# Kernel optimization log

Hardware: AMD Instinct MI355X
Metric: run time of the kernel (lower is better)

The kernel has to match this reference:

```python
import jax, jax.numpy as jnp
import numpy as np

N_NODES = 100000
N_EDGES = 1600000
NFEAT = 256
NHID = 128


def _l2_normalize(v, eps=1e-12):
    return v / (jnp.linalg.norm(v) + eps)


def setup_inputs() -> dict:
    key = jax.random.key(0)
    k1, k2, k3, k4 = jax.random.split(key, 4)
    x = jax.random.normal(k1, (N_NODES, NFEAT), dtype=jnp.float32)
    edge_index = jax.random.randint(k2, (2, N_EDGES), 0, N_NODES, dtype=jnp.int64)
    # GCNConv weight (glorot-ish scale), spectral-normalized at forward time
    W = jax.random.normal(k3, (NFEAT, NHID), dtype=jnp.float32) * 0.05
    bias = jnp.zeros((NHID,), dtype=jnp.float32)
    prelu_a = jnp.full((1,), 0.25, dtype=jnp.float32)  # nn.PReLU default slope
    u = _l2_normalize(jax.random.normal(k4, (NFEAT,), dtype=jnp.float32))
    return {"x": x, "edge_index": edge_index, "W": W, "bias": bias,
            "prelu_a": prelu_a, "u": u}


def reference(x, edge_index, W, bias, prelu_a, u):
    # --- spectral_norm: one power iteration (torch default n_power_iterations=1) ---
    v = _l2_normalize(W.T @ u)          # [NHID]
    u2 = _l2_normalize(W @ v)           # [NFEAT]
    sigma = u2 @ (W @ v)
    W_sn = W / sigma

    # --- GCNConv: linear transform, add self-loops, sym-normalize, scatter-add ---
    xw = x @ W_sn                       # [N, NHID]
    n = x.shape[0]
    loops = jnp.arange(n, dtype=edge_index.dtype)
    row = jnp.concatenate([edge_index[0], loops])  # sources
    col = jnp.concatenate([edge_index[1], loops])  # targets
    ones = jnp.ones(row.shape[0], dtype=x.dtype)
    deg = jax.ops.segment_sum(ones, col, num_segments=n)
    dinv = jnp.where(deg > 0, deg ** -0.5, 0.0)
    norm = dinv[row] * dinv[col]        # [E+N]
    msgs = norm[:, None] * xw[row]      # gather at sources
    out = jax.ops.segment_sum(msgs, col, num_segments=n) + bias

    # --- PReLU ---
    return jnp.where(out > 0, out, prelu_a * out)
```

## Files before the change

### kernel.cpp

```cpp
#include <hip/hip_runtime.h>

#define NFEAT 256
#define NHID  128

#define NBK   391
#define EPB   4096
#define NBLK  391
#define SEGW  4608

typedef __bf16 bf16x8 __attribute__((ext_vector_type(8)));
typedef __bf16 bf16x4 __attribute__((ext_vector_type(4)));
typedef float  f32x4  __attribute__((ext_vector_type(4)));

#define PIN() __builtin_amdgcn_sched_barrier(0)

__global__ __launch_bounds__(256) void sigma_kernel(const float* __restrict__ W,
                                                    const float* __restrict__ u,
                                                    float* __restrict__ scal,
                                                    int* __restrict__ bucket_fill) {
    __shared__ float v[NHID];
    __shared__ float red[256];
    int tid = threadIdx.x;

    if (tid < NBK) bucket_fill[tid] = 0;
    if (tid + 256 < NBK) bucket_fill[tid + 256] = 0;

    float t = 0.f;
    if (tid < NHID) {
        for (int i = 0; i < NFEAT; ++i) t += W[i * NHID + tid] * u[i];
    }
    red[tid] = (tid < NHID) ? t * t : 0.f;
    __syncthreads();
    for (int s = 128; s > 0; s >>= 1) {
        if (tid < s) red[tid] += red[tid + s];
        __syncthreads();
    }
    float nv = sqrtf(red[0]);
    float inv_nv = 1.f / (nv + 1e-12f);
    __syncthreads();
    if (tid < NHID) v[tid] = t * inv_nv;
    __syncthreads();

    float wv = 0.f;
    for (int j = 0; j < NHID; ++j) wv += W[tid * NHID + j] * v[j];
    red[tid] = wv * wv;
    __syncthreads();
    for (int s = 128; s > 0; s >>= 1) {
        if (tid < s) red[tid] += red[tid + s];
        __syncthreads();
    }
    if (tid == 0) {
        float n2  = red[0];
        float nwv = sqrtf(n2);
        float sigma = n2 / (nwv + 1e-12f);
        scal[0] = 1.f / sigma;
    }
}

__global__ __launch_bounds__(256) void wt_kernel(const float* __restrict__ W,
                                                 const float* __restrict__ scal,
                                                 __bf16* __restrict__ WT) {
    int idx = blockIdx.x * 256 + threadIdx.x;
    int c = idx >> 8;
    int r = idx & 255;
    WT[c * NFEAT + r] = (__bf16)(W[r * NHID + c] * scal[0]);
}

__global__ __launch_bounds__(256) void fused_kernel(const float* __restrict__ x,
                                                    const __bf16* __restrict__ WT,
                                                    __bf16* __restrict__ xwb,
                                                    const int* __restrict__ erow,
                                                    const int* __restrict__ ecol,
                                                    int* __restrict__ bucket_fill,
                                                    unsigned int* __restrict__ rbuf,
                                                    int nn, int E, int ngemm) {
    __shared__ __attribute__((aligned(16))) char sbuf[49152];

    int tid  = threadIdx.x;

    if ((int)blockIdx.x < ngemm) {
        float (*xs)[64][64] = (float (*)[64][64])sbuf;

        int lane = tid & 63;
        int w    = tid >> 6;
        int rfrag = lane & 15;
        int kg    = lane >> 4;
        int row0 = blockIdx.x * 64;

        int p16  = lane & 15;
        int rsub = lane >> 4;

        int crow0 = (w & 1) * 32 + rfrag;
        int col0  = (w >> 1) * 64;
        int r0 = row0 + crow0;
        int r1 = r0 + 16;
        const __bf16* wb = WT + (size_t)(col0 + rfrag) * NFEAT + kg * 8;
        int cr7 = crow0 & 7;

        f32x4 acc0[4] = {};
        f32x4 acc1[4] = {};

        auto STAGE = [&](int buf, int c) {
#pragma unroll
            for (int j = 0; j < 4; ++j) {
                int rloc = w * 16 + j * 4 + rsub;
                int grow = row0 + rloc;
                if (grow >= nn) grow = nn - 1;
                const float* src = x + (size_t)grow * NFEAT + c * 64 + ((p16 ^ (grow & 7)) << 2);
                __builtin_amdgcn_global_load_lds(
                    (const __attribute__((address_space(1))) void*)src,
                    (__attribute__((address_space(3))) void*)&xs[buf][w * 16 + j * 4][0],
                    16, 0, 0);
            }
        };

        bf16x8 Bf[2][2][4];
        auto BLOAD = [&](int bbuf, int c) {
#pragma unroll
            for (int ks = 0; ks < 2; ++ks)
#pragma unroll
                for (int nt = 0; nt < 4; ++nt)
                    Bf[bbuf][ks][nt] = *(const bf16x8*)(wb + (size_t)nt * 16 * NFEAT + c * 64 + ks * 32);
        };

        auto MFMA_CHUNK = [&](int buf, int bbuf) {
#pragma unroll
            for (int ks = 0; ks < 2; ++ks) {
                int sA = kg * 2 + ks * 8;
                float4 a0lo = *(const float4*)&xs[buf][crow0][((sA) ^ cr7) * 4];
                float4 a0hi = *(const float4*)&xs[buf][crow0][((sA + 1) ^ cr7) * 4];
                float4 a1lo = *(const float4*)&xs[buf][crow0 + 16][((sA) ^ cr7) * 4];
                float4 a1hi = *(const float4*)&xs[buf][crow0 + 16][((sA + 1) ^ cr7) * 4];
                bf16x8 af0, af1;
                af0[0] = (__bf16)a0lo.x; af0[1] = (__bf16)a0lo.y;
                af0[2] = (__bf16)a0lo.z; af0[3] = (__bf16)a0lo.w;
                af0[4] = (__bf16)a0hi.x; af0[5] = (__bf16)a0hi.y;
                af0[6] = (__bf16)a0hi.z; af0[7] = (__bf16)a0hi.w;
                af1[0] = (__bf16)a1lo.x; af1[1] = (__bf16)a1lo.y;
                af1[2] = (__bf16)a1lo.z; af1[3] = (__bf16)a1lo.w;
                af1[4] = (__bf16)a1hi.x; af1[5] = (__bf16)a1hi.y;
                af1[6] = (__bf16)a1hi.z; af1[7] = (__bf16)a1hi.w;
#pragma unroll
                for (int nt = 0; nt < 4; ++nt) {
                    acc0[nt] = __builtin_amdgcn_mfma_f32_16x16x32_bf16(Bf[bbuf][ks][nt], af0, acc0[nt], 0, 0, 0);
                    acc1[nt] = __builtin_amdgcn_mfma_f32_16x16x32_bf16(Bf[bbuf][ks][nt], af1, acc1[nt], 0, 0, 0);
                }
            }
        };

        STAGE(0, 0);  PIN();
        BLOAD(0, 0);  PIN();
        STAGE(1, 1);  PIN();
        asm volatile("s_waitcnt vmcnt(12)" ::: "memory");
        __builtin_amdgcn_s_barrier();

        BLOAD(1, 1);  PIN();
        STAGE(2, 2);  PIN();
        MFMA_CHUNK(0, 0);
        asm volatile("s_waitcnt vmcnt(12)" ::: "memory");
        __builtin_amdgcn_s_barrier();

        BLOAD(0, 2);  PIN();
        STAGE(0, 3);  PIN();
        MFMA_CHUNK(1, 1);
        asm volatile("s_waitcnt vmcnt(12)" ::: "memory");
        __builtin_amdgcn_s_barrier();

        BLOAD(1, 3);  PIN();
        MFMA_CHUNK(2, 0);
        asm volatile("s_waitcnt vmcnt(8)" ::: "memory");
        __builtin_amdgcn_s_barrier();

        MFMA_CHUNK(0, 1);

        if (r0 < nn) {
            __bf16* orow = xwb + (size_t)r0 * NHID + col0 + kg * 4;
#pragma unroll
            for (int nt = 0; nt < 4; ++nt) {
                bf16x4 v;
                v[0] = (__bf16)acc0[nt][0];
                v[1] = (__bf16)acc0[nt][1];
                v[2] = (__bf16)acc0[nt][2];
                v[3] = (__bf16)acc0[nt][3];
                *(bf16x4*)&orow[nt * 16] = v;
            }
        }
        if (r1 < nn) {
            __bf16* orow = xwb + (size_t)r1 * NHID + col0 + kg * 4;
#pragma unroll
            for (int nt = 0; nt < 4; ++nt) {
                bf16x4 v;
                v[0] = (__bf16)acc1[nt][0];
                v[1] = (__bf16)acc1[nt][1];
                v[2] = (__bf16)acc1[nt][2];
                v[3] = (__bf16)acc1[nt][3];
                *(bf16x4*)&orow[nt * 16] = v;
            }
        }
        return;
    }

    unsigned int*   rec   = (unsigned int*)sbuf;
    unsigned short* bkk   = (unsigned short*)(sbuf + 16384);
    int*            hist  = (int*)(sbuf + 24576);
    int*            lbase = (int*)(sbuf + 24576 + 1564);
    int*            lfill = (int*)(sbuf + 24576 + 3128);
    int*            gb    = (int*)(sbuf + 24576 + 4692);

    int b = blockIdx.x - ngemm;
    for (int k = tid; k < NBK; k += 256) { hist[k] = 0; lfill[k] = 0; }
    __syncthreads();

    int e0 = b * EPB;
    unsigned int rv[16];
    int kv[16];
#pragma unroll
    for (int j = 0; j < 16; ++j) {
        int idx = e0 + j * 256 + tid;
        if (idx < E) {
            int c = ecol[idx];
            int s = erow[idx];
            int k = c >> 8;
            kv[j] = k;
            rv[j] = ((unsigned int)(c & 255) << 24) | (unsigned int)s;
            atomicAdd(&hist[k], 1);
        } else kv[j] = -1;
    }
    __syncthreads();

    if (tid < 64) {
        int carry = 0;
        for (int c0 = 0; c0 < NBK; c0 += 64) {
            int i = c0 + tid;
            int vv = (i < NBK) ? hist[i] : 0;
            int orig = vv;
#pragma unroll
            for (int d = 1; d < 64; d <<= 1) {
                int t = __shfl_up(vv, (unsigned)d, 64);
                if (tid >= d) vv += t;
            }
            if (i < NBK) lbase[i] = carry + vv - orig;
            carry += __shfl(vv, 63, 64);
        }
    }
    __syncthreads();

    if (tid < NBK) gb[tid] = tid * SEGW + atomicAdd(&bucket_fill[tid], hist[tid]);
    if (tid + 256 < NBK) gb[tid + 256] = (tid + 256) * SEGW
                                       + atomicAdd(&bucket_fill[tid + 256], hist[tid + 256]);
    __syncthreads();

#pragma unroll
    for (int j = 0; j < 16; ++j) {
        if (kv[j] >= 0) {
            int p = lbase[kv[j]] + atomicAdd(&lfill[kv[j]], 1);
            rec[p] = rv[j];
            bkk[p] = (unsigned short)kv[j];
        }
    }
    __syncthreads();

    int nval = E - e0;
    if (nval > EPB) nval = EPB;
    for (int p = tid; p < nval; p += 256) {
        int k = bkk[p];
        rbuf[gb[k] + (p - lbase[k])] = rec[p];
    }
}

__global__ __launch_bounds__(256) void fine_kernel(const unsigned int* __restrict__ rbuf,
                                                   const int* __restrict__ bucket_fill,
                                                   int4* __restrict__ meta,
                                                   float* __restrict__ dinv,
                                                   int* __restrict__ ebuf, int n) {
    __shared__ int cnt[256], lb[256], lf[256], sc[256];
    int tid = threadIdx.x, k = blockIdx.x;
    int seg0 = k * SEGW, seg1 = seg0 + bucket_fill[k];
    cnt[tid] = 0;
    lf[tid] = 0;
    __syncthreads();
    for (int j = seg0 + tid; j < seg1; j += 256)
        atomicAdd(&cnt[rbuf[j] >> 24], 1);
    __syncthreads();
    int cv = cnt[tid];
    sc[tid] = cv;
    __syncthreads();
    int val = cv;
    for (int off = 1; off < 256; off <<= 1) {
        int t = (tid >= off) ? sc[tid - off] : 0;
        __syncthreads();
        val += t;
        sc[tid] = val;
        __syncthreads();
    }
    lb[tid] = val - cv;
    __syncthreads();
    int node = k * 256 + tid;
    if (node < n) {
        float dv = rsqrtf((float)cv + 1.f);
        int4 m;
        m.x = seg0 + lb[tid];
        m.y = cv;
        m.z = __float_as_int(dv);
        m.w = 0;
        meta[node] = m;
        dinv[node] = dv;
    }
    for (int j = seg0 + tid; j < seg1; j += 256) {
        unsigned int r = rbuf[j];
        int dl = r >> 24;
        int p = seg0 + lb[dl] + atomicAdd(&lf[dl], 1);
        ebuf[p] = (int)(r & 0xFFFFFFu);
    }
}

__global__ __launch_bounds__(256) void gather_kernel(const uint4* __restrict__ xb4,
                                                     const int4* __restrict__ meta,
                                                     const int* __restrict__ ebuf,
                                                     const float* __restrict__ dinv,
                                                     const float* __restrict__ bias,
                                                     const float* __restrict__ pa,
                                                     float* __restrict__ out, int n) {
    int tid = threadIdx.x;
    int sub = tid & 15;
    int node = (blockIdx.x * 256 + tid) >> 4;
    if (node >= n) return;

    int4 m = meta[node];
    int b = m.x, deg = m.y;
    float dn = __int_as_float(m.z);

    uint4 s0 = xb4[(size_t)node * 16 + sub];
    float a0 = dn * __uint_as_float(s0.x << 16);
    float a1 = dn * __uint_as_float(s0.x & 0xffff0000u);
    float a2 = dn * __uint_as_float(s0.y << 16);
    float a3 = dn * __uint_as_float(s0.y & 0xffff0000u);
    float a4 = dn * __uint_as_float(s0.z << 16);
    float a5 = dn * __uint_as_float(s0.z & 0xffff0000u);
    float a6 = dn * __uint_as_float(s0.w << 16);
    float a7 = dn * __uint_as_float(s0.w & 0xffff0000u);

    int k = 0;
    for (; k + 4 <= deg; k += 4) {
        int r0 = ebuf[b + k + 0];
        int r1 = ebuf[b + k + 1];
        int r2 = ebuf[b + k + 2];
        int r3 = ebuf[b + k + 3];
        float d0 = dinv[r0], d1 = dinv[r1], d2 = dinv[r2], d3 = dinv[r3];
        uint4 v0 = xb4[(size_t)r0 * 16 + sub];
        uint4 v1 = xb4[(size_t)r1 * 16 + sub];
        uint4 v2 = xb4[(size_t)r2 * 16 + sub];
        uint4 v3 = xb4[(size_t)r3 * 16 + sub];
        a0 += d0 * __uint_as_float(v0.x << 16) + d1 * __uint_as_float(v1.x << 16)
            + d2 * __uint_as_float(v2.x << 16) + d3 * __uint_as_float(v3.x << 16);
        a1 += d0 * __uint_as_float(v0.x & 0xffff0000u) + d1 * __uint_as_float(v1.x & 0xffff0000u)
            + d2 * __uint_as_float(v2.x & 0xffff0000u) + d3 * __uint_as_float(v3.x & 0xffff0000u);
        a2 += d0 * __uint_as_float(v0.y << 16) + d1 * __uint_as_float(v1.y << 16)
            + d2 * __uint_as_float(v2.y << 16) + d3 * __uint_as_float(v3.y << 16);
        a3 += d0 * __uint_as_float(v0.y & 0xffff0000u) + d1 * __uint_as_float(v1.y & 0xffff0000u)
            + d2 * __uint_as_float(v2.y & 0xffff0000u) + d3 * __uint_as_float(v3.y & 0xffff0000u);
        a4 += d0 * __uint_as_float(v0.z << 16) + d1 * __uint_as_float(v1.z << 16)
            + d2 * __uint_as_float(v2.z << 16) + d3 * __uint_as_float(v3.z << 16);
        a5 += d0 * __uint_as_float(v0.z & 0xffff0000u) + d1 * __uint_as_float(v1.z & 0xffff0000u)
            + d2 * __uint_as_float(v2.z & 0xffff0000u) + d3 * __uint_as_float(v3.z & 0xffff0000u);
        a6 += d0 * __uint_as_float(v0.w << 16) + d1 * __uint_as_float(v1.w << 16)
            + d2 * __uint_as_float(v2.w << 16) + d3 * __uint_as_float(v3.w << 16);
        a7 += d0 * __uint_as_float(v0.w & 0xffff0000u) + d1 * __uint_as_float(v1.w & 0xffff0000u)
            + d2 * __uint_as_float(v2.w & 0xffff0000u) + d3 * __uint_as_float(v3.w & 0xffff0000u);
    }
    for (; k < deg; ++k) {
        int r = ebuf[b + k];
        float d = dinv[r];
        uint4 v = xb4[(size_t)r * 16 + sub];
        a0 += d * __uint_as_float(v.x << 16);
        a1 += d * __uint_as_float(v.x & 0xffff0000u);
        a2 += d * __uint_as_float(v.y << 16);
        a3 += d * __uint_as_float(v.y & 0xffff0000u);
        a4 += d * __uint_as_float(v.z << 16);
        a5 += d * __uint_as_float(v.z & 0xffff0000u);
        a6 += d * __uint_as_float(v.w << 16);
        a7 += d * __uint_as_float(v.w & 0xffff0000u);
    }

    float alpha = pa[0];
    const float4* bb4 = (const float4*)bias;
    float4 b0 = bb4[sub * 2], b1 = bb4[sub * 2 + 1];
    float o0 = dn * a0 + b0.x;
    float o1 = dn * a1 + b0.y;
    float o2 = dn * a2 + b0.z;
    float o3 = dn * a3 + b0.w;
    float o4 = dn * a4 + b1.x;
    float o5 = dn * a5 + b1.y;
    float o6 = dn * a6 + b1.z;
    float o7 = dn * a7 + b1.w;
    o0 = o0 > 0.f ? o0 : alpha * o0;
    o1 = o1 > 0.f ? o1 : alpha * o1;
    o2 = o2 > 0.f ? o2 : alpha * o2;
    o3 = o3 > 0.f ? o3 : alpha * o3;
    o4 = o4 > 0.f ? o4 : alpha * o4;
    o5 = o5 > 0.f ? o5 : alpha * o5;
    o6 = o6 > 0.f ? o6 : alpha * o6;
    o7 = o7 > 0.f ? o7 : alpha * o7;
    float4* orow = (float4*)out + (size_t)node * 32 + sub * 2;
    orow[0] = make_float4(o0, o1, o2, o3);
    orow[1] = make_float4(o4, o5, o6, o7);
}

extern "C" void kernel_launch(void* const* d_in, const int* in_sizes, int n_in,
                              void* d_out, int out_size, void* d_ws, size_t ws_size,
                              hipStream_t stream) {
    const float* x    = (const float*)d_in[0];
    const int*   ei   = (const int*)d_in[1];
    const float* W    = (const float*)d_in[2];
    const float* bias = (const float*)d_in[3];
    const float* pa   = (const float*)d_in[4];
    const float* u    = (const float*)d_in[5];

    int n = in_sizes[0] / NFEAT;
    int e = in_sizes[1] / 2;
    const int* erow = ei;
    const int* ecol = ei + e;

    float* out = (float*)d_out;
    char* ws = (char*)d_ws;
    float*        scal   = (float*)(ws);
    int*          bfill  = (int*)  (ws + 0x0002000);
    __bf16*       WT     = (__bf16*)(ws + 0x0010000);
    float*        dinv   = (float*)(ws + 0x0100000);
    int4*         meta   = (int4*) (ws + 0x0200000);
    unsigned int* rbuf   = (unsigned int*)(ws + 0x0400000);
    int*          ebuf   = (int*)  (ws + 0x0B00000);
    __bf16*       xwb    = (__bf16*)(ws + 0x1200000);

    int ngemm = (n + 63) / 64;

    sigma_kernel<<<1, 256, 0, stream>>>(W, u, scal, bfill);
    wt_kernel<<<(NFEAT * NHID) / 256, 256, 0, stream>>>(W, scal, WT);

    fused_kernel<<<ngemm + NBLK, 256, 0, stream>>>(x, WT, xwb, erow, ecol,
                                                   bfill, rbuf, n, e, ngemm);

    fine_kernel<<<NBK, 256, 0, stream>>>(rbuf, bfill, meta, dinv, ebuf, n);

    long long gunits = (long long)n * 16;
    gather_kernel<<<(int)((gunits + 255) / 256), 256, 0, stream>>>(
        (const uint4*)xwb, meta, ebuf, dinv, bias, pa, out, n);
}
```

Baseline: 145.5 us.

## Use 128-row GEMM tiles with wave-private double-buffered 32-wide K chunks

The x@W GEMM block now covers 128 rows instead of 64. Each wave owns 32 rows across all 128 output columns, so each x row is staged once for the full output width. The three-stage, barrier-synchronised pipeline over 64-wide K chunks becomes an eight-step double-buffered loop over 32-wide K chunks. Each wave stages only the rows it reads, so the block barriers are dropped, LDS falls from 48 KB to 32 KB, and the number of GEMM blocks is halved. In exchange, every wave loads the whole W^T fragment set, raising register pressure (16 accumulators plus 8 B fragments) and W traffic per block, and the shallower prefetch may expose more load latency.

```diff
diff --git a/kernel.cpp b/kernel.cpp
--- a/kernel.cpp
+++ b/kernel.cpp
@@ -74,109 +74,89 @@
                                                     int* __restrict__ bucket_fill,
                                                     unsigned int* __restrict__ rbuf,
                                                     int nn, int E, int ngemm) {
-    __shared__ __attribute__((aligned(16))) char sbuf[49152];
+    __shared__ __attribute__((aligned(16))) char sbuf[32768];
 
     int tid  = threadIdx.x;
 
     if ((int)blockIdx.x < ngemm) {
-        float (*xs)[64][64] = (float (*)[64][64])sbuf;
+        float (*xs)[128][32] = (float (*)[128][32])sbuf;
 
         int lane = tid & 63;
         int w    = tid >> 6;
         int rfrag = lane & 15;
         int kg    = lane >> 4;
-        int row0 = blockIdx.x * 64;
-
-        int p16  = lane & 15;
-        int rsub = lane >> 4;
-
-        int crow0 = (w & 1) * 32 + rfrag;
-        int col0  = (w >> 1) * 64;
+        int row0 = blockIdx.x * 128;
+
+        int p8   = lane & 7;
+        int rsub = lane >> 3;
+
+        int crow0 = w * 32 + rfrag;
         int r0 = row0 + crow0;
         int r1 = r0 + 16;
-        const __bf16* wb = WT + (size_t)(col0 + rfrag) * NFEAT + kg * 8;
+        const __bf16* wb = WT + (size_t)rfrag * NFEAT + kg * 8;
         int cr7 = crow0 & 7;
 
-        f32x4 acc0[4] = {};
-        f32x4 acc1[4] = {};
+        f32x4 acc0[8] = {};
+        f32x4 acc1[8] = {};
 
         auto STAGE = [&](int buf, int c) {
 #pragma unroll
             for (int j = 0; j < 4; ++j) {
-                int rloc = w * 16 + j * 4 + rsub;
+                int rloc = w * 32 + j * 8 + rsub;
                 int grow = row0 + rloc;
                 if (grow >= nn) grow = nn - 1;
-                const float* src = x + (size_t)grow * NFEAT + c * 64 + ((p16 ^ (grow & 7)) << 2);
+                const float* src = x + (size_t)grow * NFEAT + c * 32 + ((p8 ^ (grow & 7)) << 2);
                 __builtin_amdgcn_global_load_lds(
                     (const __attribute__((address_space(1))) void*)src,
-                    (__attribute__((address_space(3))) void*)&xs[buf][w * 16 + j * 4][0],
+                    (__attribute__((address_space(3))) void*)&xs[buf][w * 32 + j * 8][0],
                     16, 0, 0);
             }
         };
 
-        bf16x8 Bf[2][2][4];
-        auto BLOAD = [&](int bbuf, int c) {
-#pragma unroll
-            for (int ks = 0; ks < 2; ++ks)
-#pragma unroll
-                for (int nt = 0; nt < 4; ++nt)
-                    Bf[bbuf][ks][nt] = *(const bf16x8*)(wb + (size_t)nt * 16 * NFEAT + c * 64 + ks * 32);
+        bf16x8 Bf[8];
+        auto BLOAD = [&](int c) {
+#pragma unroll
+            for (int nt = 0; nt < 8; ++nt)
+                Bf[nt] = *(const bf16x8*)(wb + (size_t)nt * 16 * NFEAT + c * 32);
         };
 
-        auto MFMA_CHUNK = [&](int buf, int bbuf) {
-#pragma unroll
-            for (int ks = 0; ks < 2; ++ks) {
-                int sA = kg * 2 + ks * 8;
-                float4 a0lo = *(const float4*)&xs[buf][crow0][((sA) ^ cr7) * 4];
-                float4 a0hi = *(const float4*)&xs[buf][crow0][((sA + 1) ^ cr7) * 4];
-                float4 a1lo = *(const float4*)&xs[buf][crow0 + 16][((sA) ^ cr7) * 4];
-                float4 a1hi = *(const float4*)&xs[buf][crow0 + 16][((sA + 1) ^ cr7) * 4];
-                bf16x8 af0, af1;
-                af0[0] = (__bf16)a0lo.x; af0[1] = (__bf16)a0lo.y;
-                af0[2] = (__bf16)a0lo.z; af0[3] = (__bf16)a0lo.w;
-                af0[4] = (__bf16)a0hi.x; af0[5] = (__bf16)a0hi.y;
-                af0[6] = (__bf16)a0hi.z; af0[7] = (__bf16)a0hi.w;
-                af1[0] = (__bf16)a1lo.x; af1[1] = (__bf16)a1lo.y;
-                af1[2] = (__bf16)a1lo.z; af1[3] = (__bf16)a1lo.w;
-                af1[4] = (__bf16)a1hi.x; af1[5] = (__bf16)a1hi.y;
-                af1[6] = (__bf16)a1hi.z; af1[7] = (__bf16)a1hi.w;
-#pragma unroll
-                for (int nt = 0; nt < 4; ++nt) {
-                    acc0[nt] = __builtin_amdgcn_mfma_f32_16x16x32_bf16(Bf[bbuf][ks][nt], af0, acc0[nt], 0, 0, 0);
-                    acc1[nt] = __builtin_amdgcn_mfma_f32_16x16x32_bf16(Bf[bbuf][ks][nt], af1, acc1[nt], 0, 0, 0);
-                }
+        auto MFMA_CHUNK = [&](int buf) {
+            int s0 = ((kg * 2) ^ cr7) * 4;
+            int s1 = ((kg * 2 + 1) ^ cr7) * 4;
+            float4 a0lo = *(const float4*)&xs[buf][crow0][s0];
+            float4 a0hi = *(const float4*)&xs[buf][crow0][s1];
+            float4 a1lo = *(const float4*)&xs[buf][crow0 + 16][s0];
+            float4 a1hi = *(const float4*)&xs[buf][crow0 + 16][s1];
+            bf16x8 af0, af1;
+            af0[0] = (__bf16)a0lo.x; af0[1] = (__bf16)a0lo.y;
+            af0[2] = (__bf16)a0lo.z; af0[3] = (__bf16)a0lo.w;
+            af0[4] = (__bf16)a0hi.x; af0[5] = (__bf16)a0hi.y;
+            af0[6] = (__bf16)a0hi.z; af0[7] = (__bf16)a0hi.w;
+            af1[0] = (__bf16)a1lo.x; af1[1] = (__bf16)a1lo.y;
+            af1[2] = (__bf16)a1lo.z; af1[3] = (__bf16)a1lo.w;
+            af1[4] = (__bf16)a1hi.x; af1[5] = (__bf16)a1hi.y;
+            af1[6] = (__bf16)a1hi.z; af1[7] = (__bf16)a1hi.w;
+#pragma unroll
+            for (int nt = 0; nt < 8; ++nt) {
+                acc0[nt] = __builtin_amdgcn_mfma_f32_16x16x32_bf16(Bf[nt], af0, acc0[nt], 0, 0, 0);
+                acc1[nt] = __builtin_amdgcn_mfma_f32_16x16x32_bf16(Bf[nt], af1, acc1[nt], 0, 0, 0);
             }
         };
 
         STAGE(0, 0);  PIN();
-        BLOAD(0, 0);  PIN();
-        STAGE(1, 1);  PIN();
-        asm volatile("s_waitcnt vmcnt(12)" ::: "memory");
-        __builtin_amdgcn_s_barrier();
-
-        BLOAD(1, 1);  PIN();
-        STAGE(2, 2);  PIN();
-        MFMA_CHUNK(0, 0);
-        asm volatile("s_waitcnt vmcnt(12)" ::: "memory");
-        __builtin_amdgcn_s_barrier();
-
-        BLOAD(0, 2);  PIN();
-        STAGE(0, 3);  PIN();
-        MFMA_CHUNK(1, 1);
-        asm volatile("s_waitcnt vmcnt(12)" ::: "memory");
-        __builtin_amdgcn_s_barrier();
-
-        BLOAD(1, 3);  PIN();
-        MFMA_CHUNK(2, 0);
-        asm volatile("s_waitcnt vmcnt(8)" ::: "memory");
-        __builtin_amdgcn_s_barrier();
-
-        MFMA_CHUNK(0, 1);
+#pragma unroll
+        for (int c = 0; c < 8; ++c) {
+            BLOAD(c);  PIN();
+            if (c < 7) { STAGE((c + 1) & 1, c + 1);  PIN(); }
+            if (c < 7) asm volatile("s_waitcnt vmcnt(4)" ::: "memory");
+            else       asm volatile("s_waitcnt vmcnt(0)" ::: "memory");
+            MFMA_CHUNK(c & 1);
+        }
 
         if (r0 < nn) {
-            __bf16* orow = xwb + (size_t)r0 * NHID + col0 + kg * 4;
-#pragma unroll
-            for (int nt = 0; nt < 4; ++nt) {
+            __bf16* orow = xwb + (size_t)r0 * NHID + kg * 4;
+#pragma unroll
+            for (int nt = 0; nt < 8; ++nt) {
                 bf16x4 v;
                 v[0] = (__bf16)acc0[nt][0];
                 v[1] = (__bf16)acc0[nt][1];
@@ -186,9 +166,9 @@
             }
         }
         if (r1 < nn) {
-            __bf16* orow = xwb + (size_t)r1 * NHID + col0 + kg * 4;
-#pragma unroll
-            for (int nt = 0; nt < 4; ++nt) {
+            __bf16* orow = xwb + (size_t)r1 * NHID + kg * 4;
+#pragma unroll
+            for (int nt = 0; nt < 8; ++nt) {
                 bf16x4 v;
                 v[0] = (__bf16)acc1[nt][0];
                 v[1] = (__bf16)acc1[nt][1];
@@ -432,7 +412,7 @@
     int*          ebuf   = (int*)  (ws + 0x0B00000);
     __bf16*       xwb    = (__bf16*)(ws + 0x1200000);
 
-    int ngemm = (n + 63) / 64;
+    int ngemm = (n + 127) / 128;
 
     sigma_kernel<<<1, 256, 0, stream>>>(W, u, scal, bfill);
     wt_kernel<<<(NFEAT * NHID) / 256, 256, 0, stream>>>(W, scal, WT);
```

New measurement: 144.3 us. About the same (-0.8%).
